# Optimization experiments

Measured on AMD Instinct MI355X. Metric: run time of the kernel, lower is better.

## Reference

```python
import jax, jax.numpy as jnp
import numpy as np

N_NODES = 50000
N_EDGES = 800000
IN_DIM = 128
HID = 128
OUT_DIM = 40
N_EXP = 4


def setup_inputs() -> dict:
    key = jax.random.key(0)
    ks = jax.random.split(key, 20)
    def lin(k, o, i, scale=None):
        s = scale if scale is not None else 1.0 / np.sqrt(i)
        return jax.random.uniform(k, (o, i), jnp.float32, -s, s)
    inp = {}
    inp['x'] = jax.random.normal(ks[0], (N_NODES, IN_DIM), jnp.float32)
    inp['edge_index'] = jax.random.randint(ks[1], (2, N_EDGES), 0, N_NODES, jnp.int64)
    # layer 0: in=IN_DIM -> HID ; layer 1: in=HID -> HID
    dims = [(IN_DIM, HID), (HID, HID)]
    for l, (ci, co) in enumerate(dims):
        inp[f'lin_w{l}'] = lin(ks[2 + 6 * l], co, ci)
        inp[f'lin_b{l}'] = jnp.zeros((co,), jnp.float32)
        inp[f'agg_w{l}'] = jax.random.uniform(ks[3 + 6 * l], (N_EXP, co, ci + co), jnp.float32, -1.0 / np.sqrt(ci + co), 1.0 / np.sqrt(ci + co))
        inp[f'agg_b{l}'] = jnp.zeros((N_EXP, co), jnp.float32)
        inp[f'gate_w{l}'] = lin(ks[4 + 6 * l], N_EXP, ci + co)
        inp[f'gate_b{l}'] = jnp.zeros((N_EXP,), jnp.float32)
    inp['post_w1'] = lin(ks[16], HID, HID)
    inp['post_b1'] = jnp.zeros((HID,), jnp.float32)
    inp['post_w2'] = lin(ks[17], OUT_DIM, HID)
    inp['post_b2'] = jnp.zeros((OUT_DIM,), jnp.float32)
    return inp


def _sage_layer(x, src, dst, lin_w, lin_b, agg_w, agg_b, gate_w, gate_b):
    n = x.shape[0]
    # message: gather source nodes, linear + relu  [E, out]
    msg = jax.nn.relu(x[src] @ lin_w.T + lin_b)
    # mean aggregation over destination nodes (empty -> 0, as in PyG)
    s = jax.ops.segment_sum(msg, dst, num_segments=n)
    cnt = jax.ops.segment_sum(jnp.ones((src.shape[0], 1), msg.dtype), dst, num_segments=n)
    aggr = s / jnp.maximum(cnt, 1.0)
    # update: gated mixture of 4 expert linears over concat(x, aggr)
    xc = jnp.concatenate([x, aggr], axis=1)            # [N, in+out]
    gate = jax.nn.softmax(xc @ gate_w.T + gate_b, axis=1)  # [N, E]
    exp = jax.nn.relu(jnp.einsum('nc,eoc->neo', xc, agg_w) + agg_b)  # [N, E, out]
    out = jnp.einsum('neo,ne->no', exp, gate)
    # F.normalize(p=2, dim=1, eps=1e-12)
    nrm = jnp.linalg.norm(out, axis=1, keepdims=True)
    return out / jnp.maximum(nrm, 1e-12)


def reference(x, edge_index,
              lin_w0, lin_b0, agg_w0, agg_b0, gate_w0, gate_b0,
              lin_w1, lin_b1, agg_w1, agg_b1, gate_w1, gate_b1,
              post_w1, post_b1, post_w2, post_b2):
    src, dst = edge_index[0], edge_index[1]
    h = _sage_layer(x, src, dst, lin_w0, lin_b0, agg_w0, agg_b0, gate_w0, gate_b0)
    h = jax.nn.relu(h)  # dropout p=0.0 -> identity
    h = _sage_layer(h, src, dst, lin_w1, lin_b1, agg_w1, agg_b1, gate_w1, gate_b1)
    h = jax.nn.relu(h)
    h = h @ post_w1.T + post_b1
    h = h @ post_w2.T + post_b2
    return jax.nn.log_softmax(h, axis=1)
```

## Files before the change

kernel.cpp:

```cpp
#include <hip/hip_runtime.h>
#include <hip/hip_bf16.h>
#include <cmath>

#define NN 50000
#define NE 800000

typedef __attribute__((ext_vector_type(4))) float f32x4;
typedef __attribute__((ext_vector_type(8))) short bfx8;

__device__ inline ushort f2bf(float x) {
  return __bfloat16_as_ushort(__float2bfloat16(x));
}

#define BAR_NODRAIN() asm volatile("s_waitcnt lgkmcnt(0)\ns_barrier" ::: "memory")

__global__ void count_kernel(const int* __restrict__ dst, unsigned int* __restrict__ cnt) {
  int e = blockIdx.x * 256 + threadIdx.x;
  if (e < NE) atomicAdd(&cnt[dst[e]], 1u);
}

__global__ void scan_kernel(unsigned int* __restrict__ cnt, unsigned int* __restrict__ rowstart) {
  __shared__ unsigned int sc[256];
  const int tid = threadIdx.x;
  const int CH = (NN + 255) / 256;
  const int beg = tid * CH;
  const int end = min(beg + CH, NN);
  unsigned int s = 0;
  for (int i = beg; i < end; ++i) s += cnt[i];
  sc[tid] = s;
  __syncthreads();
  for (int o = 1; o < 256; o <<= 1) {
    unsigned int v = (tid >= o) ? sc[tid - o] : 0u;
    __syncthreads();
    sc[tid] += v;
    __syncthreads();
  }
  unsigned int off = sc[tid] - s;
  for (int i = beg; i < end; ++i) {
    unsigned int c = cnt[i];
    rowstart[i] = off;
    cnt[i] = off;
    off += c;
  }
  if (tid == 255) rowstart[NN] = off;
}

__global__ void bucket_kernel(const int* __restrict__ src, const int* __restrict__ dst,
                              unsigned int* __restrict__ cursor, int* __restrict__ esrc) {
  int e = blockIdx.x * 256 + threadIdx.x;
  if (e < NE) {
    unsigned int pos = atomicAdd(&cursor[dst[e]], 1u);
    esrc[pos] = src[e];
  }
}

__global__ void wconv_kernel(const float* __restrict__ w, ushort* __restrict__ hi,
                             ushort* __restrict__ lo, int count) {
  int i = blockIdx.x * 256 + threadIdx.x;
  if (i < count) {
    float x = w[i];
    ushort h = f2bf(x);
    float hf = __uint_as_float(((unsigned int)h) << 16);
    hi[i] = h;
    lo[i] = f2bf(x - hf);
  }
}

__global__ __launch_bounds__(256) void aggregate_kernel(const float* __restrict__ A,
                                                        const int* __restrict__ esrc,
                                                        const unsigned int* __restrict__ rowstart,
                                                        float* __restrict__ S) {
  const int t = blockIdx.x * 256 + threadIdx.x;
  const int node = t >> 5;
  const int lane = t & 31;
  if (node >= NN) return;
  const unsigned int rs = rowstart[node], re = rowstart[node + 1];
  f32x4 acc = (f32x4){0.f, 0.f, 0.f, 0.f};
  unsigned int j = rs;
  for (; j + 4 <= re; j += 4) {
    const int s0 = esrc[j], s1 = esrc[j + 1], s2 = esrc[j + 2], s3 = esrc[j + 3];
    const f32x4 v0 = *(const f32x4*)&A[(size_t)s0 * 128 + lane * 4];
    const f32x4 v1 = *(const f32x4*)&A[(size_t)s1 * 128 + lane * 4];
    const f32x4 v2 = *(const f32x4*)&A[(size_t)s2 * 128 + lane * 4];
    const f32x4 v3 = *(const f32x4*)&A[(size_t)s3 * 128 + lane * 4];
    acc += (v0 + v1) + (v2 + v3);
  }
  for (; j < re; ++j) {
    const int s = esrc[j];
    acc += *(const f32x4*)&A[(size_t)s * 128 + lane * 4];
  }
  const float inv = 1.0f / fmaxf((float)(re - rs), 1.0f);
  *(f32x4*)&S[(size_t)node * 128 + lane * 4] = acc * inv;
}

template <int RELU>
__global__ __launch_bounds__(256, 3) void linm_kernel(const float* __restrict__ in,
                                                      const ushort* __restrict__ Whi,
                                                      const ushort* __restrict__ Wlo,
                                                      const float* __restrict__ bias,
                                                      float* __restrict__ out) {
  __shared__ __align__(16) ushort Ahi[64 * 64];
  __shared__ __align__(16) ushort Alo[64 * 64];
  __shared__ __align__(16) ushort Bhi[128 * 64];
  __shared__ __align__(16) ushort Blo[128 * 64];
  __shared__ float bs[128];

  const int tid = threadIdx.x;
  const int nb = blockIdx.x * 64;
  const int lane = tid & 63;
  const int wv = tid >> 6;
  const int cl = lane & 15;
  const int kg = lane >> 4;

  if (tid < 128) bs[tid] = bias[tid];

  f32x4 aP[4];
  bfx8 bP[2][8];

#pragma unroll
  for (int q = 0; q < 2; ++q) {
    const int task = tid + q * 256, row = task >> 3, g = task & 7;
    const int n = min(nb + row, NN - 1);
    aP[q * 2 + 0] = __builtin_nontemporal_load((const f32x4*)&in[(size_t)n * 128 + g * 8]);
    aP[q * 2 + 1] = __builtin_nontemporal_load((const f32x4*)&in[(size_t)n * 128 + g * 8 + 4]);
  }
#pragma unroll
  for (int q = 0; q < 4; ++q) {
    const int task = tid + q * 256, o = task >> 3, g = task & 7;
    bP[0][q * 2 + 0] = *(const bfx8*)&Whi[o * 128 + g * 8];
    bP[0][q * 2 + 1] = *(const bfx8*)&Wlo[o * 128 + g * 8];
  }

  f32x4 acc[4][2];
#pragma unroll
  for (int m = 0; m < 4; ++m)
#pragma unroll
    for (int f = 0; f < 2; ++f) acc[m][f] = (f32x4){0.f, 0.f, 0.f, 0.f};

#pragma unroll
  for (int c = 0; c < 2; ++c) {
    BAR_NODRAIN();
    {
#pragma unroll
      for (int q = 0; q < 2; ++q) {
        const int task = tid + q * 256, row = task >> 3, g = task & 7;
        const f32x4 v0 = aP[q * 2 + 0], v1 = aP[q * 2 + 1];
        const float vv[8] = {v0[0], v0[1], v0[2], v0[3], v1[0], v1[1], v1[2], v1[3]};
        bfx8 hv, lv;
#pragma unroll
        for (int i = 0; i < 8; ++i) {
          ushort h = f2bf(vv[i]);
          float hf = __uint_as_float(((unsigned int)h) << 16);
          hv[i] = (short)h;
          lv[i] = (short)f2bf(vv[i] - hf);
        }
        const int gsw = (g ^ (row & 7)) * 8;
        *(bfx8*)&Ahi[row * 64 + gsw] = hv;
        *(bfx8*)&Alo[row * 64 + gsw] = lv;
      }
    }
    {
#pragma unroll
      for (int q = 0; q < 4; ++q) {
        const int task = tid + q * 256, o = task >> 3, g = task & 7;
        const int gsw = (g ^ (o & 7)) * 8;
        *(bfx8*)&Bhi[o * 64 + gsw] = bP[c][q * 2 + 0];
        *(bfx8*)&Blo[o * 64 + gsw] = bP[c][q * 2 + 1];
      }
    }
    if (c == 0) {
#pragma unroll
      for (int q = 0; q < 2; ++q) {
        const int task = tid + q * 256, row = task >> 3, g = task & 7;
        const int n = min(nb + row, NN - 1);
        aP[q * 2 + 0] = __builtin_nontemporal_load((const f32x4*)&in[(size_t)n * 128 + 64 + g * 8]);
        aP[q * 2 + 1] = __builtin_nontemporal_load((const f32x4*)&in[(size_t)n * 128 + 64 + g * 8 + 4]);
      }
#pragma unroll
      for (int q = 0; q < 4; ++q) {
        const int task = tid + q * 256, o = task >> 3, g = task & 7;
        bP[1][q * 2 + 0] = *(const bfx8*)&Whi[o * 128 + 64 + g * 8];
        bP[1][q * 2 + 1] = *(const bfx8*)&Wlo[o * 128 + 64 + g * 8];
      }
    }
    BAR_NODRAIN();
#pragma unroll
    for (int ks = 0; ks < 2; ++ks) {
      bfx8 ah[4], al[4];
#pragma unroll
      for (int m = 0; m < 4; ++m) {
        const int ar = m * 16 + cl;
        const int gi = ((ks * 4 + kg) ^ (ar & 7)) * 8;
        ah[m] = *(const bfx8*)&Ahi[ar * 64 + gi];
        al[m] = *(const bfx8*)&Alo[ar * 64 + gi];
      }
#pragma unroll
      for (int f = 0; f < 2; ++f) {
        const int o = wv * 32 + f * 16 + cl;
        const int gi = ((ks * 4 + kg) ^ (o & 7)) * 8;
        const bfx8 bh = *(const bfx8*)&Bhi[o * 64 + gi];
        const bfx8 bl = *(const bfx8*)&Blo[o * 64 + gi];
#pragma unroll
        for (int m = 0; m < 4; ++m) {
          acc[m][f] = __builtin_amdgcn_mfma_f32_16x16x32_bf16(ah[m], bh, acc[m][f], 0, 0, 0);
          acc[m][f] = __builtin_amdgcn_mfma_f32_16x16x32_bf16(ah[m], bl, acc[m][f], 0, 0, 0);
          acc[m][f] = __builtin_amdgcn_mfma_f32_16x16x32_bf16(al[m], bh, acc[m][f], 0, 0, 0);
        }
      }
    }
  }

#pragma unroll
  for (int m = 0; m < 4; ++m) {
#pragma unroll
    for (int r = 0; r < 4; ++r) {
      const int node = m * 16 + kg * 4 + r;
      const int n = nb + node;
      if (n >= NN) continue;
#pragma unroll
      for (int f = 0; f < 2; ++f) {
        const int col = wv * 32 + f * 16 + cl;
        float v = acc[m][f][r] + bs[col];
        if (RELU) v = fmaxf(v, 0.f);
        out[(size_t)n * 128 + col] = v;
      }
    }
  }
}

__global__ __launch_bounds__(512, 2) void update_kernel(
    const float* __restrict__ xin, const float* __restrict__ S,
    const float* __restrict__ gw, const float* __restrict__ gb,
    const ushort* __restrict__ Whi, const ushort* __restrict__ Wlo,
    const float* __restrict__ aggb, float* __restrict__ hout) {
  __shared__ __align__(16) ushort Ahi[64 * 256];
  __shared__ __align__(16) ushort Alo[64 * 256];
  __shared__ __align__(16) ushort Bhi[128 * 64];
  __shared__ __align__(16) ushort Blo[128 * 64];
  __shared__ float wgs[1024];
  __shared__ float gbs[4];
  __shared__ float aggbs[512];
  __shared__ float gts[256];
  __shared__ float red[4 * 64];

  const int tid = threadIdx.x;
  const int nb = blockIdx.x * 64;
  const int lane = tid & 63;
  const int wv = tid >> 6;
  const int wr = wv >> 2;
  const int wc = wv & 3;
  const int cl = lane & 15;
  const int kg = lane >> 4;

  for (int i = tid; i < 1024; i += 512) wgs[i] = gw[i];
  if (tid < 512) aggbs[tid] = aggb[tid];
  if (tid < 4) gbs[tid] = gb[tid];

  const int r0 = tid >> 5;
  const int ga = tid & 31;
  f32x4 aL[4][2];
#pragma unroll
  for (int q = 0; q < 4; ++q) {
    const int row = r0 + q * 16;
    const int n = min(nb + row, NN - 1);
    const float* sp = (ga < 16) ? (xin + (size_t)n * 128 + ga * 8)
                                : (S + (size_t)n * 128 + (ga - 16) * 8);
    aL[q][0] = __builtin_nontemporal_load((const f32x4*)sp);
    aL[q][1] = __builtin_nontemporal_load((const f32x4*)(sp + 4));
  }
  bfx8 bPh[2], bPl[2];
#pragma unroll
  for (int q = 0; q < 2; ++q) {
    const int task = tid + q * 512;
    const int o = task >> 3, g = task & 7;
    bPh[q] = *(const bfx8*)&Whi[o * 256 + g * 8];
    bPl[q] = *(const bfx8*)&Wlo[o * 256 + g * 8];
  }
  __syncthreads();

  float gacc[4][4];
#pragma unroll
  for (int q = 0; q < 4; ++q)
#pragma unroll
    for (int e = 0; e < 4; ++e) gacc[q][e] = 0.f;
#pragma unroll
  for (int q = 0; q < 4; ++q) {
    const int row = r0 + q * 16;
    const f32x4 v0 = aL[q][0], v1 = aL[q][1];
    const float vv[8] = {v0[0], v0[1], v0[2], v0[3], v1[0], v1[1], v1[2], v1[3]};
    bfx8 hv, lv;
#pragma unroll
    for (int i = 0; i < 8; ++i) {
      const int k = ga * 8 + i;
#pragma unroll
      for (int e = 0; e < 4; ++e) gacc[q][e] += vv[i] * wgs[e * 256 + k];
      ushort h = f2bf(vv[i]);
      float hf = __uint_as_float(((unsigned int)h) << 16);
      hv[i] = (short)h;
      lv[i] = (short)f2bf(vv[i] - hf);
    }
    const int gsw = (ga ^ (row & 7)) * 8;
    *(bfx8*)&Ahi[row * 256 + gsw] = hv;
    *(bfx8*)&Alo[row * 256 + gsw] = lv;
  }
#pragma unroll
  for (int q = 0; q < 4; ++q) {
#pragma unroll
    for (int mask = 1; mask < 32; mask <<= 1) {
#pragma unroll
      for (int e = 0; e < 4; ++e) gacc[q][e] += __shfl_xor(gacc[q][e], mask);
    }
  }
  if ((tid & 31) == 0) {
#pragma unroll
    for (int q = 0; q < 4; ++q) {
      const int row = r0 + q * 16;
      float g0 = gacc[q][0] + gbs[0], g1 = gacc[q][1] + gbs[1];
      float g2 = gacc[q][2] + gbs[2], g3 = gacc[q][3] + gbs[3];
      float m = fmaxf(fmaxf(g0, g1), fmaxf(g2, g3));
      float e0 = expf(g0 - m), e1 = expf(g1 - m), e2 = expf(g2 - m), e3 = expf(g3 - m);
      float si = 1.0f / (e0 + e1 + e2 + e3);
      gts[row * 4 + 0] = e0 * si;
      gts[row * 4 + 1] = e1 * si;
      gts[row * 4 + 2] = e2 * si;
      gts[row * 4 + 3] = e3 * si;
    }
  }

  f32x4 res[2][2];
#pragma unroll
  for (int m = 0; m < 2; ++m)
#pragma unroll
    for (int f = 0; f < 2; ++f) res[m][f] = (f32x4){0.f, 0.f, 0.f, 0.f};

#pragma unroll
  for (int e = 0; e < 4; ++e) {
    f32x4 acc[2][2];
#pragma unroll
    for (int m = 0; m < 2; ++m)
#pragma unroll
      for (int f = 0; f < 2; ++f) acc[m][f] = (f32x4){0.f, 0.f, 0.f, 0.f};

#pragma unroll
    for (int c = 0; c < 4; ++c) {
      BAR_NODRAIN();
      {
#pragma unroll
        for (int q = 0; q < 2; ++q) {
          const int task = tid + q * 512;
          const int o = task >> 3, g = task & 7;
          const int gsw = (g ^ (o & 7)) * 8;
          *(bfx8*)&Bhi[o * 64 + gsw] = bPh[q];
          *(bfx8*)&Blo[o * 64 + gsw] = bPl[q];
        }
      }
      {
        const int pn = e * 4 + c + 1;
        if (pn < 16) {
          const int pe = pn >> 2, pc = pn & 3;
#pragma unroll
          for (int q = 0; q < 2; ++q) {
            const int task = tid + q * 512;
            const int o = task >> 3, g = task & 7;
            bPh[q] = *(const bfx8*)&Whi[pe * 32768 + o * 256 + pc * 64 + g * 8];
            bPl[q] = *(const bfx8*)&Wlo[pe * 32768 + o * 256 + pc * 64 + g * 8];
          }
        }
      }
      BAR_NODRAIN();
#pragma unroll
      for (int ks = 0; ks < 2; ++ks) {
        bfx8 ah[2], al[2];
#pragma unroll
        for (int m = 0; m < 2; ++m) {
          const int ar = wr * 32 + m * 16 + cl;
          const int gi = ((c * 8 + ks * 4 + kg) ^ (ar & 7)) * 8;
          ah[m] = *(const bfx8*)&Ahi[ar * 256 + gi];
          al[m] = *(const bfx8*)&Alo[ar * 256 + gi];
        }
#pragma unroll
        for (int f = 0; f < 2; ++f) {
          const int o = wc * 32 + f * 16 + cl;
          const int gi = ((ks * 4 + kg) ^ (o & 7)) * 8;
          const bfx8 bh = *(const bfx8*)&Bhi[o * 64 + gi];
          const bfx8 bl = *(const bfx8*)&Blo[o * 64 + gi];
#pragma unroll
          for (int m = 0; m < 2; ++m) {
            acc[m][f] = __builtin_amdgcn_mfma_f32_16x16x32_bf16(ah[m], bh, acc[m][f], 0, 0, 0);
            acc[m][f] = __builtin_amdgcn_mfma_f32_16x16x32_bf16(ah[m], bl, acc[m][f], 0, 0, 0);
            acc[m][f] = __builtin_amdgcn_mfma_f32_16x16x32_bf16(al[m], bh, acc[m][f], 0, 0, 0);
          }
        }
      }
    }
    const float b0 = aggbs[e * 128 + wc * 32 + cl];
    const float b1 = aggbs[e * 128 + wc * 32 + 16 + cl];
#pragma unroll
    for (int m = 0; m < 2; ++m) {
#pragma unroll
      for (int r = 0; r < 4; ++r) {
        const int node = wr * 32 + m * 16 + kg * 4 + r;
        const float g = gts[node * 4 + e];
        res[m][0][r] += g * fmaxf(acc[m][0][r] + b0, 0.f);
        res[m][1][r] += g * fmaxf(acc[m][1][r] + b1, 0.f);
      }
    }
  }

#pragma unroll
  for (int m = 0; m < 2; ++m) {
    f32x4 ss;
#pragma unroll
    for (int r = 0; r < 4; ++r)
      ss[r] = res[m][0][r] * res[m][0][r] + res[m][1][r] * res[m][1][r];
#pragma unroll
    for (int mask = 1; mask < 16; mask <<= 1) {
#pragma unroll
      for (int r = 0; r < 4; ++r) ss[r] += __shfl_xor(ss[r], mask);
    }
    if (cl == 0) {
#pragma unroll
      for (int r = 0; r < 4; ++r) red[wc * 64 + wr * 32 + m * 16 + kg * 4 + r] = ss[r];
    }
  }
  __syncthreads();
#pragma unroll
  for (int m = 0; m < 2; ++m) {
#pragma unroll
    for (int r = 0; r < 4; ++r) {
      const int node = wr * 32 + m * 16 + kg * 4 + r;
      const int n = nb + node;
      if (n >= NN) continue;
      const float t = red[node] + red[64 + node] + red[128 + node] + red[192 + node];
      const float inv = 1.0f / fmaxf(sqrtf(t), 1e-12f);
      hout[(size_t)n * 128 + wc * 32 + cl]      = fmaxf(res[m][0][r] * inv, 0.f);
      hout[(size_t)n * 128 + wc * 32 + 16 + cl] = fmaxf(res[m][1][r] * inv, 0.f);
    }
  }
}

__global__ void post2_kernel(const float* __restrict__ P, const float* __restrict__ W2,
                             const float* __restrict__ b2, float* __restrict__ out) {
  __shared__ __align__(16) float ps[32 * 132];
  __shared__ __align__(16) float w2s[40 * 132];
  __shared__ float b2s[40];
  const int tid = threadIdx.x;
  const int nb = blockIdx.x * 32;
  for (int i = tid; i < 5120; i += 256) {
    int o = i >> 7, k = i & 127;
    w2s[o * 132 + k] = W2[i];
  }
  if (tid < 40) b2s[tid] = b2[tid];
  {
    const int k = tid & 127;
    const int nl0 = tid >> 7;
#pragma unroll
    for (int r = 0; r < 16; ++r) {
      int nl = r * 2 + nl0;
      int n = min(nb + nl, NN - 1);
      ps[nl * 132 + k] = P[n * 128 + k];
    }
  }
  __syncthreads();

  const int nl = tid >> 3, g = tid & 7;
  float acc[5] = {0.f, 0.f, 0.f, 0.f, 0.f};
  for (int k = 0; k < 128; k += 4) {
    const float4 pv = *(const float4*)&ps[nl * 132 + k];
#pragma unroll
    for (int j = 0; j < 5; ++j) {
      const int o = g * 5 + j;
      const float4 wv = *(const float4*)&w2s[o * 132 + k];
      acc[j] += pv.x * wv.x + pv.y * wv.y + pv.z * wv.z + pv.w * wv.w;
    }
  }
  float l[5];
  float m = -1e30f;
#pragma unroll
  for (int j = 0; j < 5; ++j) {
    l[j] = acc[j] + b2s[g * 5 + j];
    m = fmaxf(m, l[j]);
  }
  m = fmaxf(m, __shfl_xor(m, 1, 8));
  m = fmaxf(m, __shfl_xor(m, 2, 8));
  m = fmaxf(m, __shfl_xor(m, 4, 8));
  float s = 0.f;
#pragma unroll
  for (int j = 0; j < 5; ++j) s += expf(l[j] - m);
  s += __shfl_xor(s, 1, 8);
  s += __shfl_xor(s, 2, 8);
  s += __shfl_xor(s, 4, 8);
  const float lse = m + logf(s);
  const int n = nb + nl;
  if (n < NN) {
#pragma unroll
    for (int j = 0; j < 5; ++j) out[n * 40 + g * 5 + j] = l[j] - lse;
  }
}

extern "C" void kernel_launch(void* const* d_in, const int* in_sizes, int n_in,
                              void* d_out, int out_size, void* d_ws, size_t ws_size,
                              hipStream_t stream) {
  const float* x       = (const float*)d_in[0];
  const int*   ei      = (const int*)d_in[1];
  const int*   src     = ei;
  const int*   dstp    = ei + NE;
  const float* lin_w0  = (const float*)d_in[2];
  const float* lin_b0  = (const float*)d_in[3];
  const float* agg_w0  = (const float*)d_in[4];
  const float* agg_b0  = (const float*)d_in[5];
  const float* gate_w0 = (const float*)d_in[6];
  const float* gate_b0 = (const float*)d_in[7];
  const float* lin_w1  = (const float*)d_in[8];
  const float* lin_b1  = (const float*)d_in[9];
  const float* agg_w1  = (const float*)d_in[10];
  const float* agg_b1  = (const float*)d_in[11];
  const float* gate_w1 = (const float*)d_in[12];
  const float* gate_b1 = (const float*)d_in[13];
  const float* post_w1 = (const float*)d_in[14];
  const float* post_b1 = (const float*)d_in[15];
  const float* post_w2 = (const float*)d_in[16];
  const float* post_b2 = (const float*)d_in[17];

  float* A  = (float*)d_ws;
  float* Sb = A + 6400000;
  float* H1 = Sb + 6400000;
  ushort* WHIa = (ushort*)(H1 + 6400000);
  ushort* WLOa = WHIa + 262144;
  ushort* WHIl = WLOa + 262144;
  ushort* WLOl = WHIl + 49152;
  unsigned int* CNT      = (unsigned int*)(WLOl + 49152);
  unsigned int* ROWSTART = CNT + NN;
  int*          ESRC     = (int*)(ROWSTART + NN + 1);

  const int gridN64 = (NN + 63) / 64;

  (void)hipMemsetAsync(CNT, 0, NN * sizeof(unsigned int), stream);
  count_kernel<<<NE / 256, 256, 0, stream>>>(dstp, CNT);
  scan_kernel<<<1, 256, 0, stream>>>(CNT, ROWSTART);
  bucket_kernel<<<NE / 256, 256, 0, stream>>>(src, dstp, CNT, ESRC);
  wconv_kernel<<<512, 256, 0, stream>>>(agg_w0, WHIa, WLOa, 131072);
  wconv_kernel<<<512, 256, 0, stream>>>(agg_w1, WHIa + 131072, WLOa + 131072, 131072);
  wconv_kernel<<<64, 256, 0, stream>>>(lin_w0, WHIl, WLOl, 16384);
  wconv_kernel<<<64, 256, 0, stream>>>(lin_w1, WHIl + 16384, WLOl + 16384, 16384);
  wconv_kernel<<<64, 256, 0, stream>>>(post_w1, WHIl + 32768, WLOl + 32768, 16384);

  linm_kernel<1><<<gridN64, 256, 0, stream>>>(x, WHIl, WLOl, lin_b0, A);
  aggregate_kernel<<<(NN * 32 + 255) / 256, 256, 0, stream>>>(A, ESRC, ROWSTART, Sb);
  update_kernel<<<gridN64, 512, 0, stream>>>(x, Sb, gate_w0, gate_b0, WHIa, WLOa, agg_b0, H1);

  linm_kernel<1><<<gridN64, 256, 0, stream>>>(H1, WHIl + 16384, WLOl + 16384, lin_b1, A);
  aggregate_kernel<<<(NN * 32 + 255) / 256, 256, 0, stream>>>(A, ESRC, ROWSTART, Sb);
  update_kernel<<<gridN64, 512, 0, stream>>>(H1, Sb, gate_w1, gate_b1, WHIa + 131072,
                                             WLOa + 131072, agg_b1, A);

  linm_kernel<0><<<gridN64, 256, 0, stream>>>(A, WHIl + 32768, WLOl + 32768, post_b1, Sb);
  post2_kernel<<<(NN + 31) / 32, 256, 0, stream>>>(Sb, post_w2, post_b2, (float*)d_out);
}
```

Baseline: 699.4 us.

## Replace single-block CSR prefix scan with three-phase multi-block scan

Measured after the change: 591.1 us. 15.5% less time.

```diff
diff --git a/kernel.cpp b/kernel.cpp
--- a/kernel.cpp
+++ b/kernel.cpp
@@ -4,6 +4,7 @@
 
 #define NN 50000
 #define NE 800000
+#define NBLK_SCAN 196
 
 typedef __attribute__((ext_vector_type(4))) float f32x4;
 typedef __attribute__((ext_vector_type(8))) short bfx8;
@@ -19,30 +20,57 @@
   if (e < NE) atomicAdd(&cnt[dst[e]], 1u);
 }
 
-__global__ void scan_kernel(unsigned int* __restrict__ cnt, unsigned int* __restrict__ rowstart) {
-  __shared__ unsigned int sc[256];
-  const int tid = threadIdx.x;
-  const int CH = (NN + 255) / 256;
-  const int beg = tid * CH;
-  const int end = min(beg + CH, NN);
-  unsigned int s = 0;
-  for (int i = beg; i < end; ++i) s += cnt[i];
-  sc[tid] = s;
+__global__ void partial_kernel(const unsigned int* __restrict__ cnt,
+                               unsigned int* __restrict__ bsum) {
+  __shared__ unsigned int s[256];
+  const int t = threadIdx.x;
+  const int i = blockIdx.x * 256 + t;
+  s[t] = (i < NN) ? cnt[i] : 0u;
+  __syncthreads();
+#pragma unroll
+  for (int o = 128; o > 0; o >>= 1) {
+    if (t < o) s[t] += s[t + o];
+    __syncthreads();
+  }
+  if (t == 0) bsum[blockIdx.x] = s[0];
+}
+
+__global__ void scanb_kernel(unsigned int* __restrict__ bsum) {
+  __shared__ unsigned int s[256];
+  const int t = threadIdx.x;
+  const unsigned int v = (t < NBLK_SCAN) ? bsum[t] : 0u;
+  s[t] = v;
   __syncthreads();
   for (int o = 1; o < 256; o <<= 1) {
-    unsigned int v = (tid >= o) ? sc[tid - o] : 0u;
+    unsigned int u = (t >= o) ? s[t - o] : 0u;
     __syncthreads();
-    sc[tid] += v;
+    s[t] += u;
     __syncthreads();
   }
-  unsigned int off = sc[tid] - s;
-  for (int i = beg; i < end; ++i) {
-    unsigned int c = cnt[i];
-    rowstart[i] = off;
-    cnt[i] = off;
-    off += c;
-  }
-  if (tid == 255) rowstart[NN] = off;
+  if (t < NBLK_SCAN) bsum[t] = s[t] - v;
+}
+
+__global__ void apply_kernel(unsigned int* __restrict__ cnt,
+                             const unsigned int* __restrict__ bsum,
+                             unsigned int* __restrict__ rowstart) {
+  __shared__ unsigned int s[256];
+  const int t = threadIdx.x;
+  const int i = blockIdx.x * 256 + t;
+  const unsigned int v = (i < NN) ? cnt[i] : 0u;
+  s[t] = v;
+  __syncthreads();
+  for (int o = 1; o < 256; o <<= 1) {
+    unsigned int u = (t >= o) ? s[t - o] : 0u;
+    __syncthreads();
+    s[t] += u;
+    __syncthreads();
+  }
+  const unsigned int excl = s[t] - v + bsum[blockIdx.x];
+  if (i < NN) {
+    rowstart[i] = excl;
+    cnt[i] = excl;
+    if (i == NN - 1) rowstart[NN] = excl + v;
+  }
 }
 
 __global__ void bucket_kernel(const int* __restrict__ src, const int* __restrict__ dst,
@@ -531,13 +559,16 @@
   ushort* WLOl = WHIl + 49152;
   unsigned int* CNT      = (unsigned int*)(WLOl + 49152);
   unsigned int* ROWSTART = CNT + NN;
-  int*          ESRC     = (int*)(ROWSTART + NN + 1);
+  unsigned int* BSUM     = ROWSTART + NN + 1;
+  int*          ESRC     = (int*)(BSUM + 256);
 
   const int gridN64 = (NN + 63) / 64;
 
   (void)hipMemsetAsync(CNT, 0, NN * sizeof(unsigned int), stream);
   count_kernel<<<NE / 256, 256, 0, stream>>>(dstp, CNT);
-  scan_kernel<<<1, 256, 0, stream>>>(CNT, ROWSTART);
+  partial_kernel<<<NBLK_SCAN, 256, 0, stream>>>(CNT, BSUM);
+  scanb_kernel<<<1, 256, 0, stream>>>(BSUM);
+  apply_kernel<<<NBLK_SCAN, 256, 0, stream>>>(CNT, BSUM, ROWSTART);
   bucket_kernel<<<NE / 256, 256, 0, stream>>>(src, dstp, CNT, ESRC);
   wconv_kernel<<<512, 256, 0, stream>>>(agg_w0, WHIa, WLOa, 131072);
   wconv_kernel<<<512, 256, 0, stream>>>(agg_w1, WHIa + 131072, WLOa + 131072, 131072);
```
